# Optimization experiments

Measured on AMD Instinct MI355X. Metric: run time of the kernel, lower is better.

Reference implementation:

```python
import jax, jax.numpy as jnp
import numpy as np

N = 100000      # nodes
E = 800000      # edges (nnz of sparse adj)
D_IN = 128      # input feature dim
H = 64          # hidden_units
EMB = 32        # embsize
N_IDX = 50000   # gathered output rows
EPS = 1e-05     # BatchNormalization epsilon


def spmm(rows, cols, vals, x):
    # out[i] = sum_{e: rows[e]==i} vals[e] * x[cols[e]]  == sparse A @ x
    return jax.ops.segment_sum(vals[:, None] * x[cols], rows, num_segments=N)


def batchnorm(x, gamma, beta):
    # training-mode BN over node (batch) axis, matching Keras BatchNormalization
    m = jnp.mean(x, axis=0)
    v = jnp.var(x, axis=0)
    return (x - m) * jax.lax.rsqrt(v + EPS) * gamma + beta


def setup_inputs() -> dict:
    key = jax.random.key(0)
    ks = jax.random.split(key, 16)
    def w(k, fan_in, shape):
        return jax.random.normal(k, shape, dtype=jnp.float32) / np.sqrt(fan_in)
    inp = {
        "features": jax.random.normal(ks[0], (N, D_IN), dtype=jnp.float32),
        "rows": jax.random.randint(ks[1], (E,), 0, N),
        "cols": jax.random.randint(ks[2], (E,), 0, N),
        "vals": jax.random.uniform(ks[3], (E,), dtype=jnp.float32),
        "idx": jax.random.randint(ks[4], (N_IDX,), 0, N),
        # layer 0 (Dense with bias since l==0)
        "Wn0": w(ks[5], D_IN, (D_IN, H)), "bn0": jnp.zeros((H,), jnp.float32),
        "Wg0": w(ks[6], D_IN, (D_IN, H)), "bg0": jnp.zeros((H,), jnp.float32),
        "ab0": jnp.zeros((H,), jnp.float32),  # BiasLayer after SpMM
        "g0": jnp.ones((H,), jnp.float32), "b0": jnp.zeros((H,), jnp.float32),
        # layer 1 (no Dense bias)
        "Wn1": w(ks[7], H, (H, H)),
        "Wg1": w(ks[8], H, (H, H)),
        "ab1": jnp.zeros((H,), jnp.float32),
        "g1": jnp.ones((H,), jnp.float32), "b1": jnp.zeros((H,), jnp.float32),
        # conv_last block (Dense use_bias=False)
        "WnL": w(ks[9], H, (H, EMB)),
        "WgL": w(ks[10], H, (H, EMB)),
        "abL": jnp.zeros((EMB,), jnp.float32),
    }
    return inp


def reference(features, rows, cols, vals, idx,
              Wn0, bn0, Wg0, bg0, ab0, g0, b0,
              Wn1, Wg1, ab1, g1, b1,
              WnL, WgL, abL):
    x = features
    # SAGE layer 0
    x_node = x @ Wn0 + bn0
    x_neigh = x @ Wg0 + bg0
    agg = spmm(rows, cols, vals, x_neigh) + ab0
    x = jax.nn.relu(batchnorm(x_node + agg, g0, b0))
    # SAGE layer 1
    x_node = x @ Wn1
    x_neigh = x @ Wg1
    agg = spmm(rows, cols, vals, x_neigh) + ab1
    x = jax.nn.relu(batchnorm(x_node + agg, g1, b1))
    # conv_last projection to embsize
    x_node = x @ WnL
    x_neigh = x @ WgL
    agg = spmm(rows, cols, vals, x_neigh) + abL
    x = x_node + agg
    return x[idx]
```

## Files before the change

### kernel.cpp

```cpp
#include <hip/hip_runtime.h>

#define NNODES 100000
#define NEDGES 800000
#define DIN    128
#define HID    64
#define EMB    32
#define NIDX   50000
#define BN_EPS 1e-5f

#define NCHK 256
#define EC   (NEDGES / NCHK)
#define NB   ((NNODES + 63) / 64)

typedef __attribute__((ext_vector_type(8))) short short8;
typedef __attribute__((ext_vector_type(4))) float f32x4;

__device__ inline unsigned short f2bf(float f) {
    unsigned u = __float_as_uint(f);
    unsigned r = u + 0x7FFFu + ((u >> 16) & 1u);
    return (unsigned short)(r >> 16);
}
__device__ inline float bf2f_lo(unsigned u) { return __uint_as_float(u << 16); }
__device__ inline float bf2f_hi(unsigned u) { return __uint_as_float(u & 0xffff0000u); }


__device__ inline void pack_seg(const float* __restrict__ Wn, const float* __restrict__ Wg,
                                unsigned short* __restrict__ Wp, int HOUT, int l2nt, int f) {
    int j = f & 7, lane = (f >> 3) & 63, g = f >> 9;
    int tt = g & ((1 << l2nt) - 1), kb = g >> l2nt;
    int k = kb * 32 + ((lane >> 4) * 8) + j;
    int nn = tt * 16 + (lane & 15);
    float v = (nn < HOUT) ? Wn[k * HOUT + nn] : Wg[k * HOUT + (nn - HOUT)];
    Wp[f] = f2bf(v);
}

__global__ void packall_k(const float* Wn0, const float* Wg0, const float* Wn1,
                          const float* Wg1, const float* WnL, const float* WgL,
                          unsigned short* Wp0, unsigned short* Wp1, unsigned short* WpL) {
    int f = blockIdx.x * 256 + threadIdx.x;
    if (f < 16384)      pack_seg(Wn0, Wg0, Wp0, 64, 3, f);
    else if (f < 24576) pack_seg(Wn1, Wg1, Wp1, 64, 3, f - 16384);
    else if (f < 28672) pack_seg(WnL, WgL, WpL, 32, 2, f - 24576);
}


__global__ __launch_bounds__(256) void bhist_k(const int* __restrict__ rows,
                                               int* __restrict__ Bcnt,
                                               const int* __restrict__ idx,
                                               int* __restrict__ mark) {
    if ((int)blockIdx.x >= NCHK) {
        int j = ((int)blockIdx.x - NCHK) * 256 + threadIdx.x;
        if (j < NIDX) mark[idx[j]] = 1;
        return;
    }
    __shared__ int hist[NB];
    int t = threadIdx.x, blk = blockIdx.x;
    for (int b = t; b < NB; b += 256) hist[b] = 0;
    __syncthreads();
    for (int i = t; i < EC; i += 256)
        atomicAdd(&hist[rows[blk * EC + i] >> 6], 1);
    __syncthreads();
    for (int b = t; b < NB; b += 256) Bcnt[b * NCHK + blk] = hist[b];
}

__global__ void bprefix_k(const int* __restrict__ Bcnt, int* __restrict__ BcntT,
                          int* __restrict__ bTot) {
    int b = blockIdx.x * 256 + threadIdx.x;
    if (b >= NB) return;
    int run = 0;
    for (int j = 0; j < NCHK; j++) {
        BcntT[j * NB + b] = run;
        run += Bcnt[b * NCHK + j];
    }
    bTot[b] = run;
}

__global__ void bscan_k(const int* __restrict__ bTot, int* __restrict__ bBase) {
    __shared__ int s[256];
    int t = threadIdx.x;
    int v[7], loc = 0;
#pragma unroll
    for (int i = 0; i < 7; i++) {
        int ix = t * 7 + i;
        v[i] = loc;
        loc += (ix < NB) ? bTot[ix] : 0;
    }
    s[t] = loc;
    __syncthreads();
    for (int off = 1; off < 256; off <<= 1) {
        int a = (t >= off) ? s[t - off] : 0;
        __syncthreads();
        s[t] += a;
        __syncthreads();
    }
    int base = s[t] - loc;
#pragma unroll
    for (int i = 0; i < 7; i++) {
        int ix = t * 7 + i;
        if (ix < NB) bBase[ix] = base + v[i];
    }
    if (t == 255) bBase[NB] = NEDGES;
}

__global__ __launch_bounds__(256) void bfinal_k(const int4* __restrict__ ebuf,
                                                const int* __restrict__ bBase,
                                                int* __restrict__ rowptr,
                                                int2* __restrict__ cs) {
    __shared__ int hist[64], sc[64], cur[64];
    int b = blockIdx.x, t = threadIdx.x;
    int e0 = bBase[b], e1 = bBase[b + 1];
    int r0 = b << 6;
    if (t < 64) hist[t] = 0;
    __syncthreads();
    for (int i = e0 + t; i < e1; i += 256)
        atomicAdd(&hist[ebuf[i].x & 63], 1);
    __syncthreads();
    if (t == 0) {
        int run = e0;
        for (int j = 0; j < 64; j++) { sc[j] = run; run += hist[j]; }
    }
    __syncthreads();
    if (t < 64) {
        cur[t] = sc[t];
        int r = r0 + t;
        if (r < NNODES) rowptr[r] = sc[t];
    }
    if (b == NB - 1 && t == 0) rowptr[NNODES] = NEDGES;
    __syncthreads();
    for (int i = e0 + t; i < e1; i += 256) {
        int4 v = ebuf[i];
        int p = atomicAdd(&cur[v.x & 63], 1);
        cs[p] = make_int2(v.y, v.z);
    }
}


template <int K, int HOUT, bool AFF, bool XBF, bool HNBF>
__device__ void gemm_body(const void* __restrict__ Xv, const unsigned short* __restrict__ Wp,
                          const float* __restrict__ bnA, const float* __restrict__ bnB,
                          const float* __restrict__ bgA,
                          const float* __restrict__ sums, const float* __restrict__ gamma,
                          const float* __restrict__ beta,
                          float* __restrict__ Hnf, unsigned short* __restrict__ Hnb,
                          unsigned short* __restrict__ Hgb, int n, int blk)
{
    constexpr int NT = 2 * HOUT / 16, NKB = K / 32;
    constexpr int RS = K + 8;
    __shared__ unsigned short Xs[64 * RS];
    __shared__ float sSc[64], sSh[64];

    const int row0 = blk * 64;
    const int t = threadIdx.x;

    if (AFF) {
        if (t < 64) {
            float sum = 0.f, sq = 0.f;
#pragma unroll
            for (int s = 0; s < 8; s++) { sum += sums[s * 128 + t]; sq += sums[s * 128 + 64 + t]; }
            float m = sum / (float)NNODES;
            float var = sq / (float)NNODES - m * m;
            float sc = gamma[t] * rsqrtf(var + BN_EPS);
            sSc[t] = sc; sSh[t] = beta[t] - m * sc;
        }
        __syncthreads();
    }

    for (int li = t; li < 64 * K / 8; li += 256) {
        int r  = li / (K / 8);
        int k8 = (li % (K / 8)) * 8;
        int rr = row0 + r;
        float v[8];
        if (XBF) {
            uint4 u = (rr < n) ? *(const uint4*)((const unsigned short*)Xv + (size_t)rr * K + k8)
                               : make_uint4(0, 0, 0, 0);
            v[0] = bf2f_lo(u.x); v[1] = bf2f_hi(u.x);
            v[2] = bf2f_lo(u.y); v[3] = bf2f_hi(u.y);
            v[4] = bf2f_lo(u.z); v[5] = bf2f_hi(u.z);
            v[6] = bf2f_lo(u.w); v[7] = bf2f_hi(u.w);
        } else {
            const float* Xf = (const float*)Xv;
            float4 a = make_float4(0.f, 0.f, 0.f, 0.f), b = a;
            if (rr < n) {
                a = *(const float4*)&Xf[(size_t)rr * K + k8];
                b = *(const float4*)&Xf[(size_t)rr * K + k8 + 4];
            }
            v[0] = a.x; v[1] = a.y; v[2] = a.z; v[3] = a.w;
            v[4] = b.x; v[5] = b.y; v[6] = b.z; v[7] = b.w;
        }
        if (AFF) {
#pragma unroll
            for (int i = 0; i < 8; i++) v[i] = fmaxf(v[i] * sSc[k8 + i] + sSh[k8 + i], 0.f);
        }
        uint4 o;
        o.x = (unsigned)f2bf(v[0]) | ((unsigned)f2bf(v[1]) << 16);
        o.y = (unsigned)f2bf(v[2]) | ((unsigned)f2bf(v[3]) << 16);
        o.z = (unsigned)f2bf(v[4]) | ((unsigned)f2bf(v[5]) << 16);
        o.w = (unsigned)f2bf(v[6]) | ((unsigned)f2bf(v[7]) << 16);
        *(uint4*)&Xs[r * RS + k8] = o;
    }
    __syncthreads();

    const int wave = t >> 6, lane = t & 63;
    const int q = lane >> 4, mrow = lane & 15;

    f32x4 acc[NT];
#pragma unroll
    for (int i = 0; i < NT; i++) acc[i] = (f32x4){0.f, 0.f, 0.f, 0.f};

    const short8* wp8 = (const short8*)Wp;
#pragma unroll
    for (int kb = 0; kb < NKB; kb++) {
        short8 a = *(const short8*)&Xs[(wave * 16 + mrow) * RS + kb * 32 + q * 8];
#pragma unroll
        for (int tt = 0; tt < NT; tt++) {
            short8 b = wp8[(kb * NT + tt) * 64 + lane];
            acc[tt] = __builtin_amdgcn_mfma_f32_16x16x32_bf16(a, b, acc[tt], 0, 0, 0);
        }
    }

#pragma unroll
    for (int tt = 0; tt < NT; tt++) {
        int nglob = tt * 16 + mrow;
        bool nside = (nglob < HOUT);
        int c = nside ? nglob : (nglob - HOUT);
        float bias = 0.f;
        if (nside) {
            if (bnA) bias += bnA[c];
            if (bnB) bias += bnB[c];
        } else if (bgA) {
            bias += bgA[c];
        }
#pragma unroll
        for (int r = 0; r < 4; r++) {
            int rr = row0 + wave * 16 + q * 4 + r;
            if (rr < n) {
                float o = acc[tt][r] + bias;
                if (nside) {
                    if (HNBF) Hnb[(size_t)rr * HOUT + c] = f2bf(o);
                    else      Hnf[(size_t)rr * HOUT + c] = o;
                } else {
                    Hgb[(size_t)rr * HOUT + c] = f2bf(o);
                }
            }
        }
    }
}

__global__ __launch_bounds__(256) void part_gemm0_k(
    const int* __restrict__ rows, const int* __restrict__ cols,
    const float* __restrict__ vals, const int* __restrict__ BcntT,
    const int* __restrict__ bBase, int4* __restrict__ ebuf,
    const float* __restrict__ X, const unsigned short* __restrict__ Wp0,
    const float* __restrict__ bn0, const float* __restrict__ ab0, const float* __restrict__ bg0,
    unsigned short* __restrict__ Hn0b, unsigned short* __restrict__ Hgb, int n)
{
    if ((int)blockIdx.x < NCHK) {
        __shared__ int cur[NB];
        int t = threadIdx.x, blk = blockIdx.x;
        for (int b = t; b < NB; b += 256) cur[b] = bBase[b] + BcntT[blk * NB + b];
        __syncthreads();
        for (int i = t; i < EC; i += 256) {
            int e = blk * EC + i;
            int r = rows[e];
            int p = atomicAdd(&cur[r >> 6], 1);
            ebuf[p] = make_int4(r, cols[e], __float_as_int(vals[e]), 0);
        }
    } else {
        gemm_body<DIN, HID, false, false, true>(X, Wp0, bn0, ab0, bg0,
            nullptr, nullptr, nullptr, nullptr, Hn0b, Hgb, n, blockIdx.x - NCHK);
    }
}

template <int K, int HOUT, bool AFF, bool XBF, bool HNBF>
__global__ __launch_bounds__(256) void gemm_k(
    const void* __restrict__ X, const unsigned short* __restrict__ Wp,
    const float* __restrict__ bnA, const float* __restrict__ bnB, const float* __restrict__ bgA,
    const float* __restrict__ sums, const float* __restrict__ gamma, const float* __restrict__ beta,
    float* __restrict__ Hnf, unsigned short* __restrict__ Hnb, unsigned short* __restrict__ Hgb, int n)
{
    gemm_body<K, HOUT, AFF, XBF, HNBF>(X, Wp, bnA, bnB, bgA, sums, gamma, beta,
                                       Hnf, Hnb, Hgb, n, blockIdx.x);
}


template <int HH, bool STATS, bool SBF, bool MARKED>
__global__ __launch_bounds__(256) void spmm_k(
    const int* __restrict__ rowptr, const int2* __restrict__ cs,
    const unsigned short* __restrict__ Hgb, void* __restrict__ Sv,
    float* __restrict__ stats, const int* __restrict__ mark, int n)
{
    constexpr int L  = HH / 4;
    constexpr int GP = 256 / L;
    const int lane = threadIdx.x % L;
    const int g = threadIdx.x / L;
    const int gid = blockIdx.x * GP + g;
    const int ngroups = gridDim.x * GP;
    const int c0 = lane * 4;

    float4 sum = make_float4(0.f, 0.f, 0.f, 0.f);
    float4 sq  = make_float4(0.f, 0.f, 0.f, 0.f);
    for (int row = gid; row < n; row += ngroups) {
        if (MARKED && !mark[row]) continue;
        int e0 = rowptr[row], e1 = rowptr[row + 1];
        float4 a0, a1 = make_float4(0.f, 0.f, 0.f, 0.f);
        if (SBF) {
            uint2 h = *(const uint2*)((const unsigned short*)Sv + (size_t)row * HH + c0);
            a0 = make_float4(bf2f_lo(h.x), bf2f_hi(h.x), bf2f_lo(h.y), bf2f_hi(h.y));
        } else {
            a0 = *(const float4*)((const float*)Sv + (size_t)row * HH + c0);
        }
        int e = e0;
        for (; e + 1 < e1; e += 2) {
            int2 p0 = cs[e], p1 = cs[e + 1];
            float v0 = __int_as_float(p0.y), v1 = __int_as_float(p1.y);
            uint2 h0 = *(const uint2*)&Hgb[(size_t)p0.x * HH + c0];
            uint2 h1 = *(const uint2*)&Hgb[(size_t)p1.x * HH + c0];
            a0.x += v0 * bf2f_lo(h0.x); a0.y += v0 * bf2f_hi(h0.x);
            a0.z += v0 * bf2f_lo(h0.y); a0.w += v0 * bf2f_hi(h0.y);
            a1.x += v1 * bf2f_lo(h1.x); a1.y += v1 * bf2f_hi(h1.x);
            a1.z += v1 * bf2f_lo(h1.y); a1.w += v1 * bf2f_hi(h1.y);
        }
        if (e < e1) {
            int2 p = cs[e];
            float v = __int_as_float(p.y);
            uint2 h = *(const uint2*)&Hgb[(size_t)p.x * HH + c0];
            a0.x += v * bf2f_lo(h.x); a0.y += v * bf2f_hi(h.x);
            a0.z += v * bf2f_lo(h.y); a0.w += v * bf2f_hi(h.y);
        }
        float4 acc = make_float4(a0.x + a1.x, a0.y + a1.y, a0.z + a1.z, a0.w + a1.w);
        if (SBF) {
            uint2 o;
            o.x = (unsigned)f2bf(acc.x) | ((unsigned)f2bf(acc.y) << 16);
            o.y = (unsigned)f2bf(acc.z) | ((unsigned)f2bf(acc.w) << 16);
            *(uint2*)((unsigned short*)Sv + (size_t)row * HH + c0) = o;
        } else {
            *(float4*)((float*)Sv + (size_t)row * HH + c0) = acc;
        }
        if (STATS) {
            sum.x += acc.x; sum.y += acc.y; sum.z += acc.z; sum.w += acc.w;
            sq.x += acc.x * acc.x; sq.y += acc.y * acc.y;
            sq.z += acc.z * acc.z; sq.w += acc.w * acc.w;
        }
    }

    if constexpr (STATS) {
        __shared__ float rs[GP][HH];
        __shared__ float rq[GP][HH];
        *(float4*)&rs[g][c0] = sum;
        *(float4*)&rq[g][c0] = sq;
        __syncthreads();
        if (threadIdx.x < HH) {
            float a = 0.f, b = 0.f;
            for (int w = 0; w < GP; w++) { a += rs[w][threadIdx.x]; b += rq[w][threadIdx.x]; }
            int stripe = blockIdx.x & 7;
            atomicAdd(&stats[stripe * 128 + threadIdx.x], a);
            atomicAdd(&stats[stripe * 128 + HH + threadIdx.x], b);
        }
    }
}

__global__ void gather_k(const float* __restrict__ S, const int* __restrict__ idx,
                         float* __restrict__ out, int total4) {
    int j = blockIdx.x * 256 + threadIdx.x;
    if (j < total4) {
        int r = j / (EMB / 4), c4 = (j % (EMB / 4)) * 4;
        *(float4*)&out[(size_t)j * 4] = *(const float4*)&S[(size_t)idx[r] * EMB + c4];
    }
}


extern "C" void kernel_launch(void* const* d_in, const int* in_sizes, int n_in,
                              void* d_out, int out_size, void* d_ws, size_t ws_size,
                              hipStream_t stream) {
    const float* features = (const float*)d_in[0];
    const int*   rows     = (const int*)d_in[1];
    const int*   cols     = (const int*)d_in[2];
    const float* vals     = (const float*)d_in[3];
    const int*   idx      = (const int*)d_in[4];
    const float* Wn0 = (const float*)d_in[5];
    const float* bn0 = (const float*)d_in[6];
    const float* Wg0 = (const float*)d_in[7];
    const float* bg0 = (const float*)d_in[8];
    const float* ab0 = (const float*)d_in[9];
    const float* g0  = (const float*)d_in[10];
    const float* b0  = (const float*)d_in[11];
    const float* Wn1 = (const float*)d_in[12];
    const float* Wg1 = (const float*)d_in[13];
    const float* ab1 = (const float*)d_in[14];
    const float* g1  = (const float*)d_in[15];
    const float* b1  = (const float*)d_in[16];
    const float* WnL = (const float*)d_in[17];
    const float* WgL = (const float*)d_in[18];
    const float* abL = (const float*)d_in[19];
    float* out = (float*)d_out;

    float*          HnLf = (float*)d_ws;
    unsigned short* nA   = (unsigned short*)(HnLf + (size_t)NNODES * EMB);
    unsigned short* nB   = nA + (size_t)NNODES * HID;
    unsigned short* Hgb  = nB + (size_t)NNODES * HID;
    int4*  ebuf  = (int4*)(Hgb + (size_t)NNODES * HID);
    int2*  cs    = (int2*)(ebuf + NEDGES);
    int*   rowptr = (int*)(cs + NEDGES);
    int*   Bcnt  = rowptr + (NNODES + 4);
    int*   BcntT = Bcnt + NB * NCHK;
    int*   bTot  = BcntT + NCHK * NB;
    int*   bBase = bTot + 1568;
    unsigned short* Wp0 = (unsigned short*)(bBase + 1568);
    unsigned short* Wp1 = Wp0 + 16384;
    unsigned short* WpL = Wp1 + 8192;
    float* stats = (float*)(WpL + 4096);
    int*   mark  = (int*)(stats + 2304);
    float* sums0 = stats;
    float* sums1 = stats + 1024;
    size_t zbytes = 2304 * 4 + (size_t)NNODES * 4;

    hipMemsetAsync(stats, 0, zbytes, stream);

    const int GBm = (NNODES + 63) / 64;
    const int MB  = (NIDX + 255) / 256;

    packall_k<<<112, 256, 0, stream>>>(Wn0, Wg0, Wn1, Wg1, WnL, WgL, Wp0, Wp1, WpL);

    bhist_k<<<NCHK + MB, 256, 0, stream>>>(rows, Bcnt, idx, mark);
    bprefix_k<<<7, 256, 0, stream>>>(Bcnt, BcntT, bTot);
    bscan_k<<<1, 256, 0, stream>>>(bTot, bBase);
    part_gemm0_k<<<NCHK + GBm, 256, 0, stream>>>(rows, cols, vals, BcntT, bBase, ebuf,
                                                 features, Wp0, bn0, ab0, bg0,
                                                 nA, Hgb, NNODES);
    bfinal_k<<<NB, 256, 0, stream>>>(ebuf, bBase, rowptr, cs);

    spmm_k<HID, true, true, false><<<1600, 256, 0, stream>>>(rowptr, cs, Hgb, nA, sums0, nullptr, NNODES);

    gemm_k<HID, HID, true, true, true><<<GBm, 256, 0, stream>>>(
        nA, Wp1, ab1, nullptr, nullptr, sums0, g0, b0, nullptr, nB, Hgb, NNODES);
    spmm_k<HID, true, true, false><<<1600, 256, 0, stream>>>(rowptr, cs, Hgb, nB, sums1, nullptr, NNODES);

    gemm_k<HID, EMB, true, true, false><<<GBm, 256, 0, stream>>>(
        nB, WpL, abL, nullptr, nullptr, sums1, g1, b1, HnLf, nullptr, Hgb, NNODES);
    spmm_k<EMB, false, false, true><<<1600, 256, 0, stream>>>(rowptr, cs, Hgb, HnLf, nullptr, mark, NNODES);

    gather_k<<<(NIDX * EMB / 4 + 255) / 256, 256, 0, stream>>>(HnLf, idx, out, NIDX * EMB / 4);
}
```

Before: 287.2 us.

## Replace CSR build with bucketed SpMM using shared-memory atomic accumulation

```diff
diff --git a/kernel.cpp b/kernel.cpp
--- a/kernel.cpp
+++ b/kernel.cpp
@@ -8,8 +8,10 @@
 #define NIDX   50000
 #define BN_EPS 1e-5f
 
-#define NCHK 256
+#define NCHK 64
 #define EC   (NEDGES / NCHK)
+#define SUBC 256
+#define ECS  (NEDGES / SUBC)
 #define NB   ((NNODES + 63) / 64)
 
 typedef __attribute__((ext_vector_type(8))) short short8;
@@ -45,11 +47,11 @@
 
 
 __global__ __launch_bounds__(256) void bhist_k(const int* __restrict__ rows,
-                                               int* __restrict__ Bcnt,
+                                               int* __restrict__ Bcnt4,
                                                const int* __restrict__ idx,
                                                int* __restrict__ mark) {
-    if ((int)blockIdx.x >= NCHK) {
-        int j = ((int)blockIdx.x - NCHK) * 256 + threadIdx.x;
+    if ((int)blockIdx.x >= SUBC) {
+        int j = ((int)blockIdx.x - SUBC) * 256 + threadIdx.x;
         if (j < NIDX) mark[idx[j]] = 1;
         return;
     }
@@ -57,20 +59,20 @@
     int t = threadIdx.x, blk = blockIdx.x;
     for (int b = t; b < NB; b += 256) hist[b] = 0;
     __syncthreads();
-    for (int i = t; i < EC; i += 256)
-        atomicAdd(&hist[rows[blk * EC + i] >> 6], 1);
-    __syncthreads();
-    for (int b = t; b < NB; b += 256) Bcnt[b * NCHK + blk] = hist[b];
-}
-
-__global__ void bprefix_k(const int* __restrict__ Bcnt, int* __restrict__ BcntT,
+    for (int i = t; i < ECS; i += 256)
+        atomicAdd(&hist[rows[blk * ECS + i] >> 6], 1);
+    __syncthreads();
+    for (int b = t; b < NB; b += 256) Bcnt4[blk * NB + b] = hist[b];
+}
+
+__global__ void bprefix_k(const int* __restrict__ Bcnt4, int* __restrict__ BcntT,
                           int* __restrict__ bTot) {
     int b = blockIdx.x * 256 + threadIdx.x;
     if (b >= NB) return;
     int run = 0;
-    for (int j = 0; j < NCHK; j++) {
-        BcntT[j * NB + b] = run;
-        run += Bcnt[b * NCHK + j];
+    for (int sub = 0; sub < SUBC; sub++) {
+        if ((sub & 3) == 0) BcntT[(sub >> 2) * NB + b] = run;
+        run += Bcnt4[sub * NB + b];
     }
     bTot[b] = run;
 }
@@ -100,38 +102,6 @@
         if (ix < NB) bBase[ix] = base + v[i];
     }
     if (t == 255) bBase[NB] = NEDGES;
-}
-
-__global__ __launch_bounds__(256) void bfinal_k(const int4* __restrict__ ebuf,
-                                                const int* __restrict__ bBase,
-                                                int* __restrict__ rowptr,
-                                                int2* __restrict__ cs) {
-    __shared__ int hist[64], sc[64], cur[64];
-    int b = blockIdx.x, t = threadIdx.x;
-    int e0 = bBase[b], e1 = bBase[b + 1];
-    int r0 = b << 6;
-    if (t < 64) hist[t] = 0;
-    __syncthreads();
-    for (int i = e0 + t; i < e1; i += 256)
-        atomicAdd(&hist[ebuf[i].x & 63], 1);
-    __syncthreads();
-    if (t == 0) {
-        int run = e0;
-        for (int j = 0; j < 64; j++) { sc[j] = run; run += hist[j]; }
-    }
-    __syncthreads();
-    if (t < 64) {
-        cur[t] = sc[t];
-        int r = r0 + t;
-        if (r < NNODES) rowptr[r] = sc[t];
-    }
-    if (b == NB - 1 && t == 0) rowptr[NNODES] = NEDGES;
-    __syncthreads();
-    for (int i = e0 + t; i < e1; i += 256) {
-        int4 v = ebuf[i];
-        int p = atomicAdd(&cur[v.x & 63], 1);
-        cs[p] = make_int2(v.y, v.z);
-    }
 }
 
 
@@ -284,77 +254,87 @@
 
 
 template <int HH, bool STATS, bool SBF, bool MARKED>
-__global__ __launch_bounds__(256) void spmm_k(
-    const int* __restrict__ rowptr, const int2* __restrict__ cs,
-    const unsigned short* __restrict__ Hgb, void* __restrict__ Sv,
-    float* __restrict__ stats, const int* __restrict__ mark, int n)
+__global__ __launch_bounds__(256) void spmmb_k(
+    const int4* __restrict__ ebuf, const int* __restrict__ bBase,
+    const unsigned short* __restrict__ Hgb, const void* __restrict__ Hn,
+    void* __restrict__ S, float* __restrict__ stats, const int* __restrict__ mark)
 {
-    constexpr int L  = HH / 4;
-    constexpr int GP = 256 / L;
-    const int lane = threadIdx.x % L;
-    const int g = threadIdx.x / L;
-    const int gid = blockIdx.x * GP + g;
-    const int ngroups = gridDim.x * GP;
-    const int c0 = lane * 4;
-
-    float4 sum = make_float4(0.f, 0.f, 0.f, 0.f);
-    float4 sq  = make_float4(0.f, 0.f, 0.f, 0.f);
-    for (int row = gid; row < n; row += ngroups) {
-        if (MARKED && !mark[row]) continue;
-        int e0 = rowptr[row], e1 = rowptr[row + 1];
-        float4 a0, a1 = make_float4(0.f, 0.f, 0.f, 0.f);
+    constexpr int L = HH / 4;
+    constexpr int G = 256 / L;
+    __shared__ float acc[64 * HH];
+    __shared__ int mk[64];
+    const int b = blockIdx.x, t = threadIdx.x;
+    const int r0 = b << 6;
+
+    for (int i = t; i < 64 * HH; i += 256) acc[i] = 0.f;
+    if (MARKED && t < 64) mk[t] = (r0 + t < NNODES) ? mark[r0 + t] : 0;
+    __syncthreads();
+
+    const int g = t / L, lane = t % L, c0 = lane * 4;
+    const int e0 = bBase[b], e1 = bBase[b + 1];
+    for (int e = e0 + g; e < e1; e += G) {
+        int4 v = ebuf[e];
+        int rl = v.x & 63;
+        if (MARKED && !mk[rl]) continue;
+        float w = __int_as_float(v.z);
+        uint2 h = *(const uint2*)&Hgb[(size_t)v.y * HH + c0];
+        float* a = &acc[rl * HH + c0];
+        atomicAdd(a + 0, w * bf2f_lo(h.x));
+        atomicAdd(a + 1, w * bf2f_hi(h.x));
+        atomicAdd(a + 2, w * bf2f_lo(h.y));
+        atomicAdd(a + 3, w * bf2f_hi(h.y));
+    }
+    __syncthreads();
+
+    constexpr int CG  = HH / 4;
+    constexpr int RPP = 256 / CG;
+    const int cg = t % CG, rl0 = t / CG, cc0 = cg * 4;
+    float4 ps = make_float4(0.f, 0.f, 0.f, 0.f);
+    float4 pq = make_float4(0.f, 0.f, 0.f, 0.f);
+    for (int pass = 0; pass < 64 / RPP; pass++) {
+        int rl = pass * RPP + rl0;
+        int rr = r0 + rl;
+        if (rr >= NNODES) break;
+        if (MARKED && !mk[rl]) continue;
+        const float* a = &acc[rl * HH + cc0];
+        float4 v;
         if (SBF) {
-            uint2 h = *(const uint2*)((const unsigned short*)Sv + (size_t)row * HH + c0);
-            a0 = make_float4(bf2f_lo(h.x), bf2f_hi(h.x), bf2f_lo(h.y), bf2f_hi(h.y));
+            uint2 h = *(const uint2*)((const unsigned short*)Hn + (size_t)rr * HH + cc0);
+            v = make_float4(a[0] + bf2f_lo(h.x), a[1] + bf2f_hi(h.x),
+                            a[2] + bf2f_lo(h.y), a[3] + bf2f_hi(h.y));
         } else {
-            a0 = *(const float4*)((const float*)Sv + (size_t)row * HH + c0);
-        }
-        int e = e0;
-        for (; e + 1 < e1; e += 2) {
-            int2 p0 = cs[e], p1 = cs[e + 1];
-            float v0 = __int_as_float(p0.y), v1 = __int_as_float(p1.y);
-            uint2 h0 = *(const uint2*)&Hgb[(size_t)p0.x * HH + c0];
-            uint2 h1 = *(const uint2*)&Hgb[(size_t)p1.x * HH + c0];
-            a0.x += v0 * bf2f_lo(h0.x); a0.y += v0 * bf2f_hi(h0.x);
-            a0.z += v0 * bf2f_lo(h0.y); a0.w += v0 * bf2f_hi(h0.y);
-            a1.x += v1 * bf2f_lo(h1.x); a1.y += v1 * bf2f_hi(h1.x);
-            a1.z += v1 * bf2f_lo(h1.y); a1.w += v1 * bf2f_hi(h1.y);
-        }
-        if (e < e1) {
-            int2 p = cs[e];
-            float v = __int_as_float(p.y);
-            uint2 h = *(const uint2*)&Hgb[(size_t)p.x * HH + c0];
-            a0.x += v * bf2f_lo(h.x); a0.y += v * bf2f_hi(h.x);
-            a0.z += v * bf2f_lo(h.y); a0.w += v * bf2f_hi(h.y);
-        }
-        float4 acc = make_float4(a0.x + a1.x, a0.y + a1.y, a0.z + a1.z, a0.w + a1.w);
+            float4 h = *(const float4*)((const float*)Hn + (size_t)rr * HH + cc0);
+            v = make_float4(a[0] + h.x, a[1] + h.y, a[2] + h.z, a[3] + h.w);
+        }
         if (SBF) {
             uint2 o;
-            o.x = (unsigned)f2bf(acc.x) | ((unsigned)f2bf(acc.y) << 16);
-            o.y = (unsigned)f2bf(acc.z) | ((unsigned)f2bf(acc.w) << 16);
-            *(uint2*)((unsigned short*)Sv + (size_t)row * HH + c0) = o;
+            o.x = (unsigned)f2bf(v.x) | ((unsigned)f2bf(v.y) << 16);
+            o.y = (unsigned)f2bf(v.z) | ((unsigned)f2bf(v.w) << 16);
+            *(uint2*)((unsigned short*)S + (size_t)rr * HH + cc0) = o;
         } else {
-            *(float4*)((float*)Sv + (size_t)row * HH + c0) = acc;
+            *(float4*)((float*)S + (size_t)rr * HH + cc0) = v;
         }
         if (STATS) {
-            sum.x += acc.x; sum.y += acc.y; sum.z += acc.z; sum.w += acc.w;
-            sq.x += acc.x * acc.x; sq.y += acc.y * acc.y;
-            sq.z += acc.z * acc.z; sq.w += acc.w * acc.w;
+            ps.x += v.x; ps.y += v.y; ps.z += v.z; ps.w += v.w;
+            pq.x += v.x * v.x; pq.y += v.y * v.y; pq.z += v.z * v.z; pq.w += v.w * v.w;
         }
     }
 
     if constexpr (STATS) {
-        __shared__ float rs[GP][HH];
-        __shared__ float rq[GP][HH];
-        *(float4*)&rs[g][c0] = sum;
-        *(float4*)&rq[g][c0] = sq;
-        __syncthreads();
-        if (threadIdx.x < HH) {
-            float a = 0.f, b = 0.f;
-            for (int w = 0; w < GP; w++) { a += rs[w][threadIdx.x]; b += rq[w][threadIdx.x]; }
-            int stripe = blockIdx.x & 7;
-            atomicAdd(&stats[stripe * 128 + threadIdx.x], a);
-            atomicAdd(&stats[stripe * 128 + HH + threadIdx.x], b);
+        __syncthreads();
+        *(float4*)&acc[t * 4] = ps;
+        *(float4*)&acc[1024 + t * 4] = pq;
+        __syncthreads();
+        if (t < 64) {
+            float s = 0.f, q = 0.f;
+            for (int rp = 0; rp < RPP; rp++) {
+                int tt = rp * CG + (t >> 2);
+                s += acc[tt * 4 + (t & 3)];
+                q += acc[1024 + tt * 4 + (t & 3)];
+            }
+            int stripe = b & 7;
+            atomicAdd(&stats[stripe * 128 + t], s);
+            atomicAdd(&stats[stripe * 128 + 64 + t], q);
         }
     }
 }
@@ -399,10 +379,8 @@
     unsigned short* nB   = nA + (size_t)NNODES * HID;
     unsigned short* Hgb  = nB + (size_t)NNODES * HID;
     int4*  ebuf  = (int4*)(Hgb + (size_t)NNODES * HID);
-    int2*  cs    = (int2*)(ebuf + NEDGES);
-    int*   rowptr = (int*)(cs + NEDGES);
-    int*   Bcnt  = rowptr + (NNODES + 4);
-    int*   BcntT = Bcnt + NB * NCHK;
+    int*   Bcnt4 = (int*)(ebuf + NEDGES);
+    int*   BcntT = Bcnt4 + SUBC * NB;
     int*   bTot  = BcntT + NCHK * NB;
     int*   bBase = bTot + 1568;
     unsigned short* Wp0 = (unsigned short*)(bBase + 1568);
@@ -421,23 +399,22 @@
 
     packall_k<<<112, 256, 0, stream>>>(Wn0, Wg0, Wn1, Wg1, WnL, WgL, Wp0, Wp1, WpL);
 
-    bhist_k<<<NCHK + MB, 256, 0, stream>>>(rows, Bcnt, idx, mark);
-    bprefix_k<<<7, 256, 0, stream>>>(Bcnt, BcntT, bTot);
+    bhist_k<<<SUBC + MB, 256, 0, stream>>>(rows, Bcnt4, idx, mark);
+    bprefix_k<<<7, 256, 0, stream>>>(Bcnt4, BcntT, bTot);
     bscan_k<<<1, 256, 0, stream>>>(bTot, bBase);
     part_gemm0_k<<<NCHK + GBm, 256, 0, stream>>>(rows, cols, vals, BcntT, bBase, ebuf,
                                                  features, Wp0, bn0, ab0, bg0,
                                                  nA, Hgb, NNODES);
-    bfinal_k<<<NB, 256, 0, stream>>>(ebuf, bBase, rowptr, cs);
-
-    spmm_k<HID, true, true, false><<<1600, 256, 0, stream>>>(rowptr, cs, Hgb, nA, sums0, nullptr, NNODES);
+
+    spmmb_k<HID, true, true, false><<<NB, 256, 0, stream>>>(ebuf, bBase, Hgb, nA, nA, sums0, nullptr);
 
     gemm_k<HID, HID, true, true, true><<<GBm, 256, 0, stream>>>(
         nA, Wp1, ab1, nullptr, nullptr, sums0, g0, b0, nullptr, nB, Hgb, NNODES);
-    spmm_k<HID, true, true, false><<<1600, 256, 0, stream>>>(rowptr, cs, Hgb, nB, sums1, nullptr, NNODES);
+    spmmb_k<HID, true, true, false><<<NB, 256, 0, stream>>>(ebuf, bBase, Hgb, nB, nB, sums1, nullptr);
 
     gemm_k<HID, EMB, true, true, false><<<GBm, 256, 0, stream>>>(
         nB, WpL, abL, nullptr, nullptr, sums1, g1, b1, HnLf, nullptr, Hgb, NNODES);
-    spmm_k<EMB, false, false, true><<<1600, 256, 0, stream>>>(rowptr, cs, Hgb, HnLf, nullptr, mark, NNODES);
+    spmmb_k<EMB, false, false, true><<<NB, 256, 0, stream>>>(ebuf, bBase, Hgb, HnLf, HnLf, nullptr, mark);
 
     gather_k<<<(NIDX * EMB / 4 + 255) / 256, 256, 0, stream>>>(HnLf, idx, out, NIDX * EMB / 4);
 }
```

Measured after the change: 903.9 us. +214.7%, slower.

## Decouple histogram sub-chunks from partition chunks to cut scatter chunk count

Applied to the files above, without the earlier changes.

```diff
diff --git a/kernel.cpp b/kernel.cpp
--- a/kernel.cpp
+++ b/kernel.cpp
@@ -8,8 +8,10 @@
 #define NIDX   50000
 #define BN_EPS 1e-5f
 
-#define NCHK 256
+#define NCHK 64
 #define EC   (NEDGES / NCHK)
+#define SUBC 256
+#define ECS  (NEDGES / SUBC)
 #define NB   ((NNODES + 63) / 64)
 
 typedef __attribute__((ext_vector_type(8))) short short8;
@@ -45,11 +47,11 @@
 
 
 __global__ __launch_bounds__(256) void bhist_k(const int* __restrict__ rows,
-                                               int* __restrict__ Bcnt,
+                                               int* __restrict__ Bcnt4,
                                                const int* __restrict__ idx,
                                                int* __restrict__ mark) {
-    if ((int)blockIdx.x >= NCHK) {
-        int j = ((int)blockIdx.x - NCHK) * 256 + threadIdx.x;
+    if ((int)blockIdx.x >= SUBC) {
+        int j = ((int)blockIdx.x - SUBC) * 256 + threadIdx.x;
         if (j < NIDX) mark[idx[j]] = 1;
         return;
     }
@@ -57,20 +59,20 @@
     int t = threadIdx.x, blk = blockIdx.x;
     for (int b = t; b < NB; b += 256) hist[b] = 0;
     __syncthreads();
-    for (int i = t; i < EC; i += 256)
-        atomicAdd(&hist[rows[blk * EC + i] >> 6], 1);
-    __syncthreads();
-    for (int b = t; b < NB; b += 256) Bcnt[b * NCHK + blk] = hist[b];
-}
-
-__global__ void bprefix_k(const int* __restrict__ Bcnt, int* __restrict__ BcntT,
+    for (int i = t; i < ECS; i += 256)
+        atomicAdd(&hist[rows[blk * ECS + i] >> 6], 1);
+    __syncthreads();
+    for (int b = t; b < NB; b += 256) Bcnt4[blk * NB + b] = hist[b];
+}
+
+__global__ void bprefix_k(const int* __restrict__ Bcnt4, int* __restrict__ BcntT,
                           int* __restrict__ bTot) {
     int b = blockIdx.x * 256 + threadIdx.x;
     if (b >= NB) return;
     int run = 0;
-    for (int j = 0; j < NCHK; j++) {
-        BcntT[j * NB + b] = run;
-        run += Bcnt[b * NCHK + j];
+    for (int sub = 0; sub < SUBC; sub++) {
+        if ((sub & 3) == 0) BcntT[(sub >> 2) * NB + b] = run;
+        run += Bcnt4[sub * NB + b];
     }
     bTot[b] = run;
 }
@@ -401,8 +403,8 @@
     int4*  ebuf  = (int4*)(Hgb + (size_t)NNODES * HID);
     int2*  cs    = (int2*)(ebuf + NEDGES);
     int*   rowptr = (int*)(cs + NEDGES);
-    int*   Bcnt  = rowptr + (NNODES + 4);
-    int*   BcntT = Bcnt + NB * NCHK;
+    int*   Bcnt4 = rowptr + (NNODES + 4);
+    int*   BcntT = Bcnt4 + SUBC * NB;
     int*   bTot  = BcntT + NCHK * NB;
     int*   bBase = bTot + 1568;
     unsigned short* Wp0 = (unsigned short*)(bBase + 1568);
@@ -421,8 +423,8 @@
 
     packall_k<<<112, 256, 0, stream>>>(Wn0, Wg0, Wn1, Wg1, WnL, WgL, Wp0, Wp1, WpL);
 
-    bhist_k<<<NCHK + MB, 256, 0, stream>>>(rows, Bcnt, idx, mark);
-    bprefix_k<<<7, 256, 0, stream>>>(Bcnt, BcntT, bTot);
+    bhist_k<<<SUBC + MB, 256, 0, stream>>>(rows, Bcnt4, idx, mark);
+    bprefix_k<<<7, 256, 0, stream>>>(Bcnt4, BcntT, bTot);
     bscan_k<<<1, 256, 0, stream>>>(bTot, bBase);
     part_gemm0_k<<<NCHK + GBm, 256, 0, stream>>>(rows, cols, vals, BcntT, bBase, ebuf,
                                                  features, Wp0, bn0, ab0, bg0,
```

After: 303.0 us. 5.5% more time.
